# Kernel optimization log

Hardware: AMD Instinct MI355X
Metric: run time of the kernel (lower is better)

The kernel has to match this reference:

```python
import math
import jax, jax.numpy as jnp
import numpy as np

B, H, W = 2, 128, 128
HW = H * W
D, NH, NL, KS = 256, 8, 1, 5
NP = KS * KS
HD = D // NH
DFF = 1024
KEEP = 0.25
H_SIZE = 188.0
EPS = 1e-5


def _layernorm(x, g, b):
    m = x.mean(-1, keepdims=True)
    v = ((x - m) ** 2).mean(-1, keepdims=True)
    return (x - m) * jax.lax.rsqrt(v + EPS) * g + b


def _mha(q_in, k_in, v_in, w_qkv, b_qkv, w_o, b_o):
    wq, wk, wv = jnp.split(w_qkv, 3, axis=0)
    bq, bk, bv = jnp.split(b_qkv, 3, axis=0)
    def heads(x, w, b):
        y = x @ w.T + b
        return y.reshape(y.shape[0], y.shape[1], NH, HD)
    q, k, v = heads(q_in, wq, bq), heads(k_in, wk, bk), heads(v_in, wv, bv)
    scores = jnp.einsum('bqhd,bkhd->bhqk', q, k) / math.sqrt(HD)
    attn = jax.nn.softmax(scores, axis=-1)
    out = jnp.einsum('bhqk,bkhd->bqhd', attn, v).reshape(q_in.shape[0], q_in.shape[1], D)
    return out @ w_o.T + b_o


def _bilinear(v, grid):
    # v: (B, HW, NH, HD); grid: (B, LQ, NH, NP, 2) normalized (x, y) in [0,1]
    x = grid[..., 0] * W - 0.5
    y = grid[..., 1] * H - 0.5
    x0 = jnp.floor(x); y0 = jnp.floor(y)
    lx = x - x0; ly = y - y0
    x0i = x0.astype(jnp.int32); y0i = y0.astype(jnp.int32)
    bidx = jnp.arange(v.shape[0])[:, None, None, None]
    hidx = jnp.arange(NH)[None, None, :, None]
    def corner(xi, yi, wgt):
        valid = (xi >= 0) & (xi < W) & (yi >= 0) & (yi < H)  # zero-pad outside
        idx = jnp.clip(yi, 0, H - 1) * W + jnp.clip(xi, 0, W - 1)
        s = v[bidx, idx, hidx]  # (B, LQ, NH, NP, HD)
        return s * (wgt * valid)[..., None]
    return (corner(x0i, y0i, (1 - lx) * (1 - ly))
            + corner(x0i + 1, y0i, lx * (1 - ly))
            + corner(x0i, y0i + 1, (1 - lx) * ly)
            + corner(x0i + 1, y0i + 1, lx * ly))


def _where_to_attend(query, ref_windows, lbw, lbb, sow, sob, kernel_indices):
    Bq, L = ref_windows.shape[:2]
    ob = (query @ lbw.T + lbb).reshape(Bq, L, NH, NL, 4)  # with_rotation=False -> 4 vars
    rw = ref_windows[:, :, None, None, :]  # (B, L, 1, 1, 7)
    ref_boxes = rw[..., jnp.array([0, 1, 3, 4])]
    ref_angles = rw[..., 6:7]
    angles = jnp.broadcast_to(ref_angles, (Bq, L, NH, NL, 1))
    boxes = ref_boxes + ob / 8.0 * ref_boxes[..., jnp.array([2, 3, 2, 3])]
    center = boxes[..., None, :2]  # (B, L, NH, NL, 1, 2)
    size = boxes[..., None, 2:]
    cos_a, sin_a = jnp.cos(angles), jnp.sin(angles)
    rot = jnp.stack([cos_a, -sin_a, sin_a, cos_a], -1).reshape(Bq, L, NH, NL, 1, 2, 2)
    dgrid = (query @ sow.T + sob).reshape(Bq, L, NH, NL, NP, 2) / H_SIZE
    fg = kernel_indices * jax.nn.relu(size)              # (B, L, NH, NL, NP, 2)
    fg = center + (fg[..., None, :] * rot).sum(-1)       # rotate then shift
    return fg + dgrid


def _box_attn(query, value, ref_windows, vpw, vpb, law, lab, lbw, lbb, sow, sob, ow, ob_, kernel_indices):
    Bq, LQ = query.shape[:2]
    LV = value.shape[1]
    v = (value @ vpw.T + vpb).reshape(Bq, LV, NH, HD)
    aw = jax.nn.softmax((query @ law.T + lab).reshape(Bq, LQ, NH, NL * NP), axis=-1)
    aw = aw.reshape(Bq, LQ, NH, NL, NP)
    grid = _where_to_attend(query, ref_windows, lbw, lbb, sow, sob, kernel_indices)
    sampled = _bilinear(v, grid[:, :, :, 0])             # single level (NL=1)
    out = (aw[:, :, :, 0, :, None] * sampled).sum(-2).reshape(Bq, LQ, D)
    return out @ ow.T + ob_


def _forward(src, pos, ref_windows, score_mask, in_proj_w, in_proj_b, mha_out_w, mha_out_b,
             value_proj_w, value_proj_b, linear_attn_w, linear_attn_b, linear_box_w, linear_box_b,
             samp_off_w, samp_off_b, ca_out_w, ca_out_b, lin1_w, lin1_b, lin2_w, lin2_b,
             qn_g, qn_b, n1_g, n1_b, n2_g, n2_b, kernel_indices):
    Bq = src.shape[0]
    fg_num = math.ceil(src.shape[1] * KEEP)
    sel_score, indices = jax.lax.top_k(score_mask, fg_num)
    gather = lambda x, i: jnp.take_along_axis(x, i[..., None], axis=1)
    sel_src = gather(src, indices)
    sel_pos = gather(pos, indices)
    sel_ref = gather(ref_windows, indices)
    q_num = math.ceil(fg_num * KEEP)
    q_idx = jax.lax.top_k(sel_score, q_num)[1]
    q_src = gather(sel_src, q_idx)
    q_pos = gather(sel_pos, q_idx)
    qk = q_src + q_pos
    q2 = _mha(qk, qk, q_src, in_proj_w, in_proj_b, mha_out_w, mha_out_b)
    q_src = _layernorm(q_src + q2, qn_g, qn_b)
    brow = jnp.arange(Bq)[:, None]
    sel_src = sel_src.at[brow, q_idx].set(q_src)
    src2 = _box_attn(sel_src + sel_pos, src, sel_ref, value_proj_w, value_proj_b,
                     linear_attn_w, linear_attn_b, linear_box_w, linear_box_b,
                     samp_off_w, samp_off_b, ca_out_w, ca_out_b, kernel_indices)
    sel_src = _layernorm(sel_src + src2, n1_g, n1_b)
    ff = jax.nn.relu(sel_src @ lin1_w.T + lin1_b) @ lin2_w.T + lin2_b
    sel_src = _layernorm(sel_src + ff, n2_g, n2_b)
    return src.at[brow, indices].set(sel_src)


def setup_inputs() -> dict:
    key = jax.random.key(0)
    ks = jax.random.split(key, 16)
    def w(k, shape):
        return jax.random.normal(k, shape, dtype=jnp.float32) * 0.02
    # deformable sampling-offsets bias init (per-head directional grid)
    thetas = np.arange(NH) * (2.0 * np.pi / NH)
    g = np.stack([np.cos(thetas), np.sin(thetas)], -1)
    g = g / np.abs(g).max(-1, keepdims=True)
    g = np.tile(g.reshape(NH, 1, 1, 2), (1, NL, NP, 1)) * (np.arange(NP) + 1).reshape(1, 1, NP, 1)
    samp_off_b = jnp.asarray(g.reshape(-1), dtype=jnp.float32)
    # fixed kernel indices buffer (odd kernel, (x,y) order, /kernel_size)
    ind = np.linspace(-(KS - 1) / 2, (KS - 1) / 2, KS)
    ii, jj = np.meshgrid(ind, ind, indexing='ij')
    kernel_indices = jnp.asarray(np.stack([jj, ii], -1).reshape(-1, 2) / KS, dtype=jnp.float32)
    return dict(
        src=jax.random.normal(ks[0], (B, HW, D), dtype=jnp.float32),
        pos=jax.random.normal(ks[1], (B, HW, D), dtype=jnp.float32),
        src_shape=jnp.array([[H, W]], dtype=jnp.int32),
        src_start_idx=jnp.zeros((1,), dtype=jnp.int32),
        ref_windows=jax.random.uniform(ks[2], (B, HW, 7), dtype=jnp.float32),
        score_mask=jax.random.normal(ks[3], (B, HW), dtype=jnp.float32),
        in_proj_w=w(ks[4], (3 * D, D)), in_proj_b=jnp.zeros((3 * D,), jnp.float32),
        mha_out_w=w(ks[5], (D, D)), mha_out_b=jnp.zeros((D,), jnp.float32),
        value_proj_w=w(ks[6], (D, D)), value_proj_b=jnp.zeros((D,), jnp.float32),
        linear_attn_w=w(ks[7], (NH * NL * NP, D)), linear_attn_b=jnp.zeros((NH * NL * NP,), jnp.float32),
        linear_box_w=w(ks[8], (NL * NH * 4, D)), linear_box_b=jnp.zeros((NL * NH * 4,), jnp.float32),
        samp_off_w=w(ks[9], (NH * NL * NP * 2, D)), samp_off_b=samp_off_b,
        ca_out_w=w(ks[10], (D, D)), ca_out_b=jnp.zeros((D,), jnp.float32),
        lin1_w=w(ks[11], (DFF, D)), lin1_b=jnp.zeros((DFF,), jnp.float32),
        lin2_w=w(ks[12], (D, DFF)), lin2_b=jnp.zeros((D,), jnp.float32),
        qn_g=jnp.ones((D,), jnp.float32), qn_b=jnp.zeros((D,), jnp.float32),
        n1_g=jnp.ones((D,), jnp.float32), n1_b=jnp.zeros((D,), jnp.float32),
        n2_g=jnp.ones((D,), jnp.float32), n2_b=jnp.zeros((D,), jnp.float32),
        kernel_indices=kernel_indices,
    )


def reference(src, pos, src_shape, src_start_idx, ref_windows, score_mask,
              in_proj_w, in_proj_b, mha_out_w, mha_out_b, value_proj_w, value_proj_b,
              linear_attn_w, linear_attn_b, linear_box_w, linear_box_b, samp_off_w, samp_off_b,
              ca_out_w, ca_out_b, lin1_w, lin1_b, lin2_w, lin2_b,
              qn_g, qn_b, n1_g, n1_b, n2_g, n2_b, kernel_indices):
    # src_shape/src_start_idx are static single-level metadata (H, W closed over)
    return _forward(src, pos, ref_windows, score_mask, in_proj_w, in_proj_b, mha_out_w, mha_out_b,
                    value_proj_w, value_proj_b, linear_attn_w, linear_attn_b, linear_box_w, linear_box_b,
                    samp_off_w, samp_off_b, ca_out_w, ca_out_b, lin1_w, lin1_b, lin2_w, lin2_b,
                    qn_g, qn_b, n1_g, n1_b, n2_g, n2_b, kernel_indices)
```

## Files before the change

kernel.cpp:

```cpp
#include <hip/hip_runtime.h>
#include <hip/hip_bf16.h>
#include <math.h>

#define HW_N   16384
#define DIM    256
#define NSEL   4096
#define NQ     1024
#define NHEAD  8
#define HD     32
#define NP_    25
#define DFF_   1024

#define OFF_SELREF  8448LL
#define OFF_SELSRC  65792LL
#define OFF_SELPOS  2162944LL
#define OFF_QUERY   4260096LL
#define OFF_BIG     6357248LL
#define OFF_WBF     10551552LL
#define OFF_F       14745856LL

__device__ __forceinline__ unsigned int f2s(float f) {
    unsigned int u = __float_as_uint(f);
    return (u & 0x80000000u) ? ~u : (u | 0x80000000u);
}

typedef __bf16 bf16x8 __attribute__((ext_vector_type(8)));
typedef __bf16 bf16x4 __attribute__((ext_vector_type(4)));
typedef float  f32x4  __attribute__((ext_vector_type(4)));

extern "C" __global__ __launch_bounds__(256)
void wcvt_kernel(const float* __restrict__ s0, const float* __restrict__ s1,
                 const float* __restrict__ s2, const float* __restrict__ s3,
                 const float* __restrict__ s4, const float* __restrict__ s5,
                 const float* __restrict__ s6, const float* __restrict__ s7,
                 const float* __restrict__ s8, __hip_bfloat16* __restrict__ dst) {
    const long long g = (long long)blockIdx.x * 256 + threadIdx.x;
    const float* s; long long base;
    if      (g < 196608)  { s = s0; base = 0; }
    else if (g < 262144)  { s = s1; base = 196608; }
    else if (g < 327680)  { s = s2; base = 262144; }
    else if (g < 378880)  { s = s3; base = 327680; }
    else if (g < 387072)  { s = s4; base = 378880; }
    else if (g < 489472)  { s = s5; base = 387072; }
    else if (g < 555008)  { s = s6; base = 489472; }
    else if (g < 817152)  { s = s7; base = 555008; }
    else                  { s = s8; base = 817152; }
    dst[g] = __float2bfloat16(s[g - base]);
}

extern "C" __global__ __launch_bounds__(512)
void topk_hist_kernel(const float* __restrict__ score, unsigned int* __restrict__ hist) {
    const int t = threadIdx.x, bx = blockIdx.x, bb = blockIdx.y;
    const int i = bx * 512 + t;
    unsigned int u = f2s(score[(long long)bb * HW_N + i]);
    atomicAdd(&hist[bb * 8192 + (u >> 19)], 1u);
}

extern "C" __global__ __launch_bounds__(1024)
void topk_scan_kernel(const unsigned int* __restrict__ hist, unsigned int* __restrict__ ctrl) {
    __shared__ unsigned int scan[1024];
    const int t = threadIdx.x, bb = blockIdx.x;
    unsigned int loc[8]; unsigned int lsum = 0u;
    #pragma unroll
    for (int k = 0; k < 8; ++k) { loc[k] = hist[bb * 8192 + t * 8 + k]; lsum += loc[k]; }
    scan[t] = lsum;
    __syncthreads();
    for (int off = 1; off < 1024; off <<= 1) {
        unsigned int v = (t + off < 1024) ? scan[t + off] : 0u;
        __syncthreads();
        scan[t] += v;
        __syncthreads();
    }
    unsigned int nxt = (t < 1023) ? scan[t + 1] : 0u;
    unsigned int run = nxt;
    for (int k = 7; k >= 0; --k) {
        run += loc[k];
        unsigned int above = run - loc[k];
        if (run >= 1024u && above < 1024u) { ctrl[bb * 16 + 0] = (unsigned)(t * 8 + k); ctrl[bb * 16 + 1] = 1024u - above; }
        if (run >= 4096u && above < 4096u) { ctrl[bb * 16 + 2] = (unsigned)(t * 8 + k); ctrl[bb * 16 + 3] = 4096u - above; }
    }
}

extern "C" __global__ __launch_bounds__(1024)
void topk_collect_kernel(const float* __restrict__ score, unsigned int* __restrict__ ctrl,
                         unsigned long long* __restrict__ list1,
                         unsigned long long* __restrict__ list2) {
    const int t = threadIdx.x, bx = blockIdx.x, bb = blockIdx.y;
    const int i = bx * 1024 + t;
    const unsigned int T1 = ctrl[bb * 16 + 0], T2 = ctrl[bb * 16 + 2];
    unsigned int u = f2s(score[(long long)bb * HW_N + i]);
    unsigned int bin = u >> 19;
    unsigned long long key = ((unsigned long long)u << 32) | (unsigned int)(~(unsigned int)i);
    if (bin == T1) {
        unsigned int p = atomicAdd(&ctrl[bb * 16 + 4], 1u);
        if (p < 2048u) list1[bb * 2048 + p] = key;
    }
    if (bin == T2 && T2 != T1) {
        unsigned int p = atomicAdd(&ctrl[bb * 16 + 5], 1u);
        if (p < 2048u) list2[bb * 2048 + p] = key;
    }
}

extern "C" __global__ __launch_bounds__(1024)
void topk_classify_kernel(const float* __restrict__ score, unsigned int* __restrict__ ctrl,
                          const unsigned long long* __restrict__ list1,
                          const unsigned long long* __restrict__ list2,
                          int* __restrict__ idx_out) {
    __shared__ unsigned int cA, cB, baseA, baseB;
    const int t = threadIdx.x, bx = blockIdx.x, bb = blockIdx.y;
    const int i = bx * 1024 + t;
    if (t == 0) { cA = 0u; cB = 0u; }
    __syncthreads();
    const unsigned int T1 = ctrl[bb * 16 + 0], need1 = ctrl[bb * 16 + 1];
    const unsigned int T2 = ctrl[bb * 16 + 2], need2 = ctrl[bb * 16 + 3];
    const unsigned int c1 = min(ctrl[bb * 16 + 4], 2048u);
    const unsigned int c2 = min(ctrl[bb * 16 + 5], 2048u);
    unsigned int u = f2s(score[(long long)bb * HW_N + i]);
    unsigned int bin = u >> 19;
    unsigned long long key = ((unsigned long long)u << 32) | (unsigned int)(~(unsigned int)i);
    bool inA = false, inB = false;
    if (bin > T1) {
        inA = true;
    } else if (bin == T1) {
        unsigned int r = 0;
        for (unsigned int q = 0; q < c1; ++q) r += (list1[bb * 2048 + q] > key) ? 1u : 0u;
        if (r < need1) inA = true;
        else if (T2 == T1) inB = (r < need2);
        else inB = true;
    } else if (bin > T2) {
        inB = true;
    } else if (bin == T2) {
        unsigned int r = 0;
        for (unsigned int q = 0; q < c2; ++q) r += (list2[bb * 2048 + q] > key) ? 1u : 0u;
        inB = (r < need2);
    }
    unsigned int sA = 0u, sB = 0u;
    if (inA) sA = atomicAdd(&cA, 1u);
    if (inB) sB = atomicAdd(&cB, 1u);
    __syncthreads();
    if (t == 0) {
        baseA = atomicAdd(&ctrl[bb * 16 + 6], cA);
        baseB = atomicAdd(&ctrl[bb * 16 + 7], cB);
    }
    __syncthreads();
    if (inA) idx_out[bb * NSEL + baseA + sA] = i;
    if (inB) idx_out[bb * NSEL + 1024 + baseB + sB] = i;
}

extern "C" __global__ __launch_bounds__(256)
void gather_kernel(const float* __restrict__ src, const float* __restrict__ pos,
                   const float* __restrict__ refw, const int* __restrict__ idx,
                   float* __restrict__ selsrc, float* __restrict__ selpos,
                   float* __restrict__ selref, float* __restrict__ qk) {
    const int s = blockIdx.x, bb = blockIdx.y, t = threadIdx.x;
    const int i = idx[bb * NSEL + s];
    const long long so = ((long long)(bb * NSEL + s)) * DIM;
    const long long go = ((long long)(bb * HW_N + i)) * DIM;
    float sv = src[go + t], pv = pos[go + t];
    selsrc[so + t] = sv;
    selpos[so + t] = pv;
    if (s < NQ) qk[((long long)(bb * NQ + s)) * DIM + t] = sv + pv;
    if (t < 7)
        selref[(long long)(bb * NSEL + s) * 7 + t] = refw[(long long)(bb * HW_N + i) * 7 + t];
}

extern "C" __global__ __launch_bounds__(256)
void gemm_kernel(const void* __restrict__ Avp, long long sA,
                 const __hip_bfloat16* __restrict__ W, const float* __restrict__ bias,
                 float* __restrict__ C, long long sC,
                 int M, int N, int K, int relu, int omode, int amode) {
    __shared__ __hip_bfloat16 As[64][72];
    __shared__ __hip_bfloat16 Ws[64][72];
    const int t = threadIdx.x;
    const int n0 = blockIdx.x * 64, m0 = blockIdx.y * 64;
    const long long zoff = (long long)blockIdx.z * sC;
    const int lane = t & 63, wv = t >> 6;
    const int mw = (wv >> 1) * 32, nw = (wv & 1) * 32;
    const int fr = lane & 15;
    const int fk = (lane >> 4) * 8;
    const int sr = t >> 2;
    const int sk = (t & 3) * 16;

    f32x4 acc[2][2];
    #pragma unroll
    for (int i = 0; i < 2; ++i)
        #pragma unroll
        for (int j = 0; j < 2; ++j) acc[i][j] = {0.f, 0.f, 0.f, 0.f};

    const bool wok = (n0 + sr) < N;
    for (int k0 = 0; k0 < K; k0 += 64) {
        uint4 wa = make_uint4(0u, 0u, 0u, 0u), wb = make_uint4(0u, 0u, 0u, 0u);
        if (wok) {
            const __hip_bfloat16* wp = W + (long long)(n0 + sr) * K + k0 + sk;
            wa = *(const uint4*)wp;
            wb = *(const uint4*)(wp + 8);
        }
        if (amode) {
            const __hip_bfloat16* ap = (const __hip_bfloat16*)Avp
                + (long long)blockIdx.z * sA + (long long)(m0 + sr) * K + k0 + sk;
            uint4 aa = *(const uint4*)ap;
            uint4 ab = *(const uint4*)(ap + 8);
            __syncthreads();
            *(uint4*)&As[sr][sk] = aa;
            *(uint4*)&As[sr][sk + 8] = ab;
            *(uint4*)&Ws[sr][sk] = wa;
            *(uint4*)&Ws[sr][sk + 8] = wb;
        } else {
            const float* ap = (const float*)Avp
                + (long long)blockIdx.z * sA + (long long)(m0 + sr) * K + k0 + sk;
            float av[16];
            #pragma unroll
            for (int q = 0; q < 4; ++q) {
                float4 v = *(const float4*)(ap + q * 4);
                av[q * 4 + 0] = v.x; av[q * 4 + 1] = v.y; av[q * 4 + 2] = v.z; av[q * 4 + 3] = v.w;
            }
            __syncthreads();
            #pragma unroll
            for (int q = 0; q < 16; ++q) As[sr][sk + q] = __float2bfloat16(av[q]);
            *(uint4*)&Ws[sr][sk] = wa;
            *(uint4*)&Ws[sr][sk + 8] = wb;
        }
        __syncthreads();
        #pragma unroll
        for (int kk = 0; kk < 64; kk += 32) {
            bf16x8 a0 = *(const bf16x8*)&As[mw + fr][kk + fk];
            bf16x8 a1 = *(const bf16x8*)&As[mw + 16 + fr][kk + fk];
            bf16x8 b0 = *(const bf16x8*)&Ws[nw + fr][kk + fk];
            bf16x8 b1 = *(const bf16x8*)&Ws[nw + 16 + fr][kk + fk];
            acc[0][0] = __builtin_amdgcn_mfma_f32_16x16x32_bf16(a0, b0, acc[0][0], 0, 0, 0);
            acc[0][1] = __builtin_amdgcn_mfma_f32_16x16x32_bf16(a0, b1, acc[0][1], 0, 0, 0);
            acc[1][0] = __builtin_amdgcn_mfma_f32_16x16x32_bf16(a1, b0, acc[1][0], 0, 0, 0);
            acc[1][1] = __builtin_amdgcn_mfma_f32_16x16x32_bf16(a1, b1, acc[1][1], 0, 0, 0);
        }
    }
    const int crow = (lane >> 4) * 4;
    #pragma unroll
    for (int mi = 0; mi < 2; ++mi) {
        #pragma unroll
        for (int ni = 0; ni < 2; ++ni) {
            const int col = n0 + nw + ni * 16 + fr;
            if (col < N) {
                const float bv = bias ? bias[col] : 0.f;
                #pragma unroll
                for (int r = 0; r < 4; ++r) {
                    const int row = m0 + mw + mi * 16 + crow + r;
                    float v = acc[mi][ni][r] + bv;
                    if (relu) v = fmaxf(v, 0.f);
                    if (omode == 0) {
                        C[zoff + (long long)row * N + col] = v;
                    } else if (omode == 1) {
                        ((__hip_bfloat16*)C)[zoff + (long long)row * N + col] = __float2bfloat16(v);
                    } else if (omode == 2) {
                        ((__hip_bfloat16*)C)[zoff + (long long)col * M + row] = __float2bfloat16(v);
                    } else {
                        ((__hip_bfloat16*)C)[zoff + ((long long)(col >> 5) * 16384 + row) * 32 + (col & 31)]
                            = __float2bfloat16(v);
                    }
                }
            }
        }
    }
}

extern "C" __global__ __launch_bounds__(256, 4)
void attn_kernel(const __hip_bfloat16* __restrict__ qkb,
                 const __hip_bfloat16* __restrict__ vT,
                 float* __restrict__ attout) {
    __shared__ float sbuf[8256];
    __shared__ float redm[4][16];
    __shared__ float reds[4][16];
    __hip_bfloat16 (*pb)[1032] = (__hip_bfloat16 (*)[1032])sbuf;
    float (*redo)[16][33] = (float (*)[16][33])sbuf;
    const int t = threadIdx.x;
    const int qt = blockIdx.x, h = blockIdx.y, bb = blockIdx.z;
    const int q0 = qt * 16;
    const int lane = t & 63, wv = t >> 6;
    const int fr = lane & 15, g = lane >> 4;
    const int kbase = wv * 256;
    const float scale = 0.17677669529663687f;

    bf16x8 qfrag = *(const bf16x8*)(qkb + ((long long)(bb * NQ + q0 + fr)) * 512 + h * HD + g * 8);

    f32x4 sfr[16];
    #pragma unroll
    for (int half = 0; half < 2; ++half) {
        bf16x8 kf[8];
        #pragma unroll
        for (int j = 0; j < 8; ++j) {
            const int key0 = kbase + (half * 8 + j) * 16;
            kf[j] = *(const bf16x8*)(qkb + ((long long)(bb * NQ + key0 + fr)) * 512 + 256 + h * HD + g * 8);
        }
        __builtin_amdgcn_sched_barrier(0);
        #pragma unroll
        for (int j = 0; j < 8; ++j) {
            f32x4 z = {0.f, 0.f, 0.f, 0.f};
            sfr[half * 8 + j] = __builtin_amdgcn_mfma_f32_16x16x32_bf16(qfrag, kf[j], z, 0, 0, 0);
        }
    }
    #pragma unroll
    for (int kt = 0; kt < 16; ++kt)
        #pragma unroll
        for (int r = 0; r < 4; ++r) sfr[kt][r] *= scale;

    float mxr[4];
    #pragma unroll
    for (int r = 0; r < 4; ++r) {
        float mx = -1e30f;
        #pragma unroll
        for (int kt = 0; kt < 16; ++kt) mx = fmaxf(mx, sfr[kt][r]);
        #pragma unroll
        for (int mm = 1; mm <= 8; mm <<= 1) mx = fmaxf(mx, __shfl_xor(mx, mm, 64));
        float sm = 0.f;
        #pragma unroll
        for (int kt = 0; kt < 16; ++kt) {
            float e = __expf(sfr[kt][r] - mx);
            sfr[kt][r] = e;
            sm += e;
        }
        #pragma unroll
        for (int mm = 1; mm <= 8; mm <<= 1) sm += __shfl_xor(sm, mm, 64);
        mxr[r] = mx;
        if (fr == 0) { redm[wv][4 * g + r] = mx; reds[wv][4 * g + r] = sm; }
    }
    __syncthreads();

    float scl[4];
    #pragma unroll
    for (int r = 0; r < 4; ++r) {
        const int q = 4 * g + r;
        float mm = fmaxf(fmaxf(redm[0][q], redm[1][q]), fmaxf(redm[2][q], redm[3][q]));
        float ll = 0.f;
        #pragma unroll
        for (int w2 = 0; w2 < 4; ++w2) ll += reds[w2][q] * __expf(redm[w2][q] - mm);
        scl[r] = __expf(mxr[r] - mm) / ll;
    }
    #pragma unroll
    for (int kt = 0; kt < 16; ++kt) {
        #pragma unroll
        for (int r = 0; r < 4; ++r) {
            pb[4 * g + r][kbase + kt * 16 + fr] = __float2bfloat16(sfr[kt][r] * scl[r]);
        }
    }

    f32x4 o0 = {0.f, 0.f, 0.f, 0.f}, o1 = {0.f, 0.f, 0.f, 0.f};
    const __hip_bfloat16* vbase = vT + ((long long)bb * DIM + h * HD) * 1024;
    #pragma unroll
    for (int ksb = 0; ksb < 2; ++ksb) {
        bf16x8 pf[4], v0[4], v1[4];
        #pragma unroll
        for (int j = 0; j < 4; ++j) {
            const int key0 = kbase + (ksb * 4 + j) * 32 + g * 8;
            pf[j] = *(const bf16x8*)&pb[fr][key0];
            v0[j] = *(const bf16x8*)(vbase + (long long)fr * 1024 + key0);
            v1[j] = *(const bf16x8*)(vbase + (long long)(16 + fr) * 1024 + key0);
        }
        __builtin_amdgcn_sched_barrier(0);
        #pragma unroll
        for (int j = 0; j < 4; ++j) {
            o0 = __builtin_amdgcn_mfma_f32_16x16x32_bf16(pf[j], v0[j], o0, 0, 0, 0);
            o1 = __builtin_amdgcn_mfma_f32_16x16x32_bf16(pf[j], v1[j], o1, 0, 0, 0);
        }
    }

    __syncthreads();
    #pragma unroll
    for (int r = 0; r < 4; ++r) {
        redo[wv][4 * g + r][fr] = o0[r];
        redo[wv][4 * g + r][16 + fr] = o1[r];
    }
    __syncthreads();
    #pragma unroll
    for (int i = 0; i < 2; ++i) {
        const int idx = t + i * 256;
        const int q = idx >> 5, d = idx & 31;
        float v = redo[0][q][d] + redo[1][q][d] + redo[2][q][d] + redo[3][q][d];
        attout[((long long)(bb * NQ + q0 + q)) * DIM + h * HD + d] = v;
    }
}

extern "C" __global__ __launch_bounds__(256)
void ln_kernel(const float* __restrict__ X, long long sx,
               const float* __restrict__ R, long long sr,
               const float* __restrict__ g, const float* __restrict__ bta,
               float* __restrict__ O, long long so) {
    __shared__ float red[4];
    const int row = blockIdx.x, bb = blockIdx.y, t = threadIdx.x;
    float x = X[(long long)bb * sx + (long long)row * DIM + t]
            + R[(long long)bb * sr + (long long)row * DIM + t];
    float v = x;
    #pragma unroll
    for (int m = 32; m >= 1; m >>= 1) v += __shfl_xor(v, m, 64);
    if ((t & 63) == 0) red[t >> 6] = v;
    __syncthreads();
    float mean = (red[0] + red[1] + red[2] + red[3]) * (1.f / 256.f);
    __syncthreads();
    float d = x - mean;
    v = d * d;
    #pragma unroll
    for (int m = 32; m >= 1; m >>= 1) v += __shfl_xor(v, m, 64);
    if ((t & 63) == 0) red[t >> 6] = v;
    __syncthreads();
    float var = (red[0] + red[1] + red[2] + red[3]) * (1.f / 256.f);
    O[(long long)bb * so + (long long)row * DIM + t] = d * rsqrtf(var + 1e-5f) * g[t] + bta[t];
}

extern "C" __global__ __launch_bounds__(256)
void addq_kernel(const float* __restrict__ a, const float* __restrict__ b2, float* __restrict__ o) {
    long long i = (long long)blockIdx.x * 256 + threadIdx.x;
    o[i] = a[i] + b2[i];
}

extern "C" __global__ __launch_bounds__(256)
void boxattn_kernel(const float* __restrict__ aw, const float* __restrict__ ob,
                    const float* __restrict__ dgrid, const float* __restrict__ selref,
                    const __hip_bfloat16* __restrict__ vp, const float* __restrict__ kidx,
                    float* __restrict__ boxout) {
    __shared__ float aw_s[200];
    __shared__ float ob_s[32];
    __shared__ float ref_s[7];
    __shared__ float ki_s[50];
    __shared__ float box_s[8][6];
    __shared__ float mx_s[8];
    __shared__ float inv_s[8];
    __shared__ float wq_s[200];
    __shared__ int   i4_s[800];
    __shared__ float w4_s[800];
    __shared__ float red4[4][8][33];
    const int t = threadIdx.x;
    const int s = blockIdx.x, bb = blockIdx.y;
    const long long base = (long long)(bb * NSEL + s);
    if (t < 200) aw_s[t] = aw[base * 200 + t];
    if (t < 32)  ob_s[t] = ob[base * 32 + t];
    if (t < 7)   ref_s[t] = selref[base * 7 + t];
    if (t < 50)  ki_s[t] = kidx[t];
    __syncthreads();

    if (t < 8) {
        float mx = -1e30f;
        #pragma unroll
        for (int p = 0; p < NP_; ++p) mx = fmaxf(mx, aw_s[t * NP_ + p]);
        mx_s[t] = mx;
        const float r0 = ref_s[0], r1 = ref_s[1], r3 = ref_s[3], r4 = ref_s[4], r6 = ref_s[6];
        box_s[t][0] = r0 + ob_s[t * 4 + 0] * 0.125f * r3;
        box_s[t][1] = r1 + ob_s[t * 4 + 1] * 0.125f * r4;
        box_s[t][2] = fmaxf(r3 + ob_s[t * 4 + 2] * 0.125f * r3, 0.f);
        box_s[t][3] = fmaxf(r4 + ob_s[t * 4 + 3] * 0.125f * r4, 0.f);
        box_s[t][4] = cosf(r6);
        box_s[t][5] = sinf(r6);
    }
    __syncthreads();

    if (t < 200) {
        const int h = t / NP_, p = t - h * NP_;
        const float w = expf(aw_s[t] - mx_s[h]);
        wq_s[t] = w;
        const float cx = box_s[h][0], cy = box_s[h][1];
        const float sw = box_s[h][2], sh = box_s[h][3];
        const float ca = box_s[h][4], sa = box_s[h][5];
        const float fx = ki_s[p * 2 + 0] * sw;
        const float fy = ki_s[p * 2 + 1] * sh;
        const float gx = cx + ca * fx - sa * fy + dgrid[base * 400 + 2 * t + 0] * (1.f / 188.f);
        const float gy = cy + sa * fx + ca * fy + dgrid[base * 400 + 2 * t + 1] * (1.f / 188.f);
        const float x = gx * 128.f - 0.5f;
        const float y = gy * 128.f - 0.5f;
        const float x0f = floorf(x), y0f = floorf(y);
        const float lx = x - x0f, ly = y - y0f;
        const int x0 = (int)x0f, y0 = (int)y0f;
        #pragma unroll
        for (int c = 0; c < 4; ++c) {
            const int xi = x0 + (c & 1);
            const int yi = y0 + (c >> 1);
            const float wgt = ((c & 1) ? lx : 1.f - lx) * ((c >> 1) ? ly : 1.f - ly);
            const bool valid = (xi >= 0) & (xi < 128) & (yi >= 0) & (yi < 128);
            const int cxi = min(max(xi, 0), 127);
            const int cyi = min(max(yi, 0), 127);
            i4_s[t * 4 + c] = cyi * 128 + cxi;
            w4_s[t * 4 + c] = w * (valid ? wgt : 0.f);
        }
    }
    __syncthreads();
    if (t < 8) {
        float sm = 0.f;
        #pragma unroll
        for (int p = 0; p < NP_; ++p) sm += wq_s[t * NP_ + p];
        inv_s[t] = 1.f / sm;
    }

    {
        const int lane = t & 63, wv = t >> 6;
        const int h2 = lane >> 3;
        const int j2 = (lane >> 2) & 1;
        const int q2 = lane & 3;
        const int stream = wv * 2 + j2;
        const __hip_bfloat16* vb = vp + ((long long)(bb * 8 + h2) * 16384) * 32 + q2 * 8;
        float a[8] = {0.f, 0.f, 0.f, 0.f, 0.f, 0.f, 0.f, 0.f};
        #pragma unroll
        for (int u = 0; u < 13; ++u) {
            const int j = stream + u * 8;
            const bool ok = (j < 100);
            const int e = h2 * 100 + (ok ? j : 0);
            bf16x8 v = *(const bf16x8*)(vb + (long long)i4_s[e] * 32);
            const float w = ok ? w4_s[e] : 0.f;
            #pragma unroll
            for (int k = 0; k < 8; ++k) a[k] += w * (float)v[k];
        }
        #pragma unroll
        for (int k = 0; k < 8; ++k) a[k] += __shfl_xor(a[k], 4, 64);
        if (j2 == 0) {
            #pragma unroll
            for (int k = 0; k < 8; ++k) red4[wv][h2][q2 * 8 + k] = a[k];
        }
    }
    __syncthreads();
    {
        const int h = t >> 5, d = t & 31;
        float v = red4[0][h][d] + red4[1][h][d] + red4[2][h][d] + red4[3][h][d];
        boxout[base * DIM + h * HD + d] = v * inv_s[h];
    }
}

extern "C" __global__ __launch_bounds__(256)
void scatter_kernel(const int* __restrict__ idx, const float* __restrict__ sel,
                    float* __restrict__ out) {
    const int s = blockIdx.x, bb = blockIdx.y, t = threadIdx.x;
    const int i = idx[bb * NSEL + s];
    out[((long long)(bb * HW_N + i)) * DIM + t] = sel[((long long)(bb * NSEL + s)) * DIM + t];
}

extern "C" void kernel_launch(void* const* d_in, const int* in_sizes, int n_in,
                              void* d_out, int out_size, void* d_ws, size_t ws_size,
                              hipStream_t stream) {
    const float* src          = (const float*)d_in[0];
    const float* pos          = (const float*)d_in[1];
    const float* refw         = (const float*)d_in[4];
    const float* score        = (const float*)d_in[5];
    const float* in_proj_w    = (const float*)d_in[6];
    const float* in_proj_b    = (const float*)d_in[7];
    const float* mha_out_w    = (const float*)d_in[8];
    const float* mha_out_b    = (const float*)d_in[9];
    const float* value_proj_w = (const float*)d_in[10];
    const float* value_proj_b = (const float*)d_in[11];
    const float* lin_attn_w   = (const float*)d_in[12];
    const float* lin_attn_b   = (const float*)d_in[13];
    const float* lin_box_w    = (const float*)d_in[14];
    const float* lin_box_b    = (const float*)d_in[15];
    const float* samp_off_w   = (const float*)d_in[16];
    const float* samp_off_b   = (const float*)d_in[17];
    const float* ca_out_w     = (const float*)d_in[18];
    const float* ca_out_b     = (const float*)d_in[19];
    const float* lin1_w       = (const float*)d_in[20];
    const float* lin1_b       = (const float*)d_in[21];
    const float* lin2_w       = (const float*)d_in[22];
    const float* lin2_b       = (const float*)d_in[23];
    const float* qn_g         = (const float*)d_in[24];
    const float* qn_b         = (const float*)d_in[25];
    const float* n1_g         = (const float*)d_in[26];
    const float* n1_b         = (const float*)d_in[27];
    const float* n2_g         = (const float*)d_in[28];
    const float* n2_b         = (const float*)d_in[29];
    const float* kidx         = (const float*)d_in[30];

    float* w = (float*)d_ws;
    int* idxp = (int*)d_ws;
    float* selref = w + OFF_SELREF;
    float* selsrc = w + OFF_SELSRC;
    float* selpos = w + OFF_SELPOS;
    float* boxout = w + OFF_SELPOS;
    float* query  = w + OFF_QUERY;
    float* src2   = w + OFF_QUERY;
    __hip_bfloat16* vproj  = (__hip_bfloat16*)(w + OFF_BIG);
    __hip_bfloat16* ffntb  = (__hip_bfloat16*)(w + OFF_BIG);
    __hip_bfloat16* wbf    = (__hip_bfloat16*)(w + OFF_WBF);
    float* qk     = w + OFF_F;
    __hip_bfloat16* qkb = (__hip_bfloat16*)(w + OFF_F + 524288);
    __hip_bfloat16* vT  = (__hip_bfloat16*)(w + OFF_F + 1572864);
    float* attout = w + OFF_F + 2097152;
    float* q2     = w + OFF_F + 2621440;
    float* aw     = w + OFF_F;
    float* obuf   = w + OFF_F + 1638400;
    float* dgrid  = w + OFF_F + 1900544;
    float* ff     = w + OFF_F;
    unsigned int* hist2 = (unsigned int*)(w + OFF_F);
    unsigned int* ctrl2 = hist2 + 16384;
    unsigned long long* list1 = (unsigned long long*)(hist2 + 16448);
    unsigned long long* list2 = list1 + 2 * 2048;
    float* out    = (float*)d_out;

    const long long W_INPROJ = 0, W_MHAOUT = 196608, W_VALUE = 262144,
                    W_LATTN = 327680, W_LBOX = 378880, W_SOFF = 387072,
                    W_CAOUT = 489472, W_LIN1 = 555008, W_LIN2 = 817152;

    hipMemcpyAsync(d_out, src, (size_t)2 * HW_N * DIM * sizeof(float),
                   hipMemcpyDeviceToDevice, stream);

    wcvt_kernel<<<4216, 256, 0, stream>>>(in_proj_w, mha_out_w, value_proj_w,
                                          lin_attn_w, lin_box_w, samp_off_w,
                                          ca_out_w, lin1_w, lin2_w, wbf);

    hipMemsetAsync(hist2, 0, 16448 * sizeof(unsigned int), stream);
    topk_hist_kernel<<<dim3(32, 2), 512, 0, stream>>>(score, hist2);
    topk_scan_kernel<<<2, 1024, 0, stream>>>(hist2, ctrl2);
    topk_collect_kernel<<<dim3(16, 2), 1024, 0, stream>>>(score, ctrl2, list1, list2);
    topk_classify_kernel<<<dim3(16, 2), 1024, 0, stream>>>(score, ctrl2, list1, list2, idxp);

    gather_kernel<<<dim3(NSEL, 2), 256, 0, stream>>>(src, pos, refw, idxp,
                                                     selsrc, selpos, selref, qk);
    gemm_kernel<<<dim3(8, 16, 2), 256, 0, stream>>>(qk, 262144LL, wbf + W_INPROJ, in_proj_b,
                                                    (float*)qkb, 524288LL, NQ, 512, 256, 0, 1, 0);
    gemm_kernel<<<dim3(4, 16, 2), 256, 0, stream>>>(selsrc, 1048576LL, wbf + W_INPROJ + 512 * 256,
                                                    in_proj_b + 512, (float*)vT, 262144LL, NQ, 256, 256, 0, 2, 0);
    attn_kernel<<<dim3(64, 8, 2), 256, 0, stream>>>(qkb, vT, attout);
    gemm_kernel<<<dim3(4, 16, 2), 256, 0, stream>>>(attout, 262144LL, wbf + W_MHAOUT, mha_out_b,
                                                    q2, 262144LL, NQ, 256, 256, 0, 0, 0);
    ln_kernel<<<dim3(NQ, 2), 256, 0, stream>>>(selsrc, 1048576LL, q2, 262144LL,
                                               qn_g, qn_b, selsrc, 1048576LL);
    addq_kernel<<<8192, 256, 0, stream>>>(selsrc, selpos, query);
    gemm_kernel<<<dim3(4, 256, 2), 256, 0, stream>>>(src, 4194304LL, wbf + W_VALUE, value_proj_b,
                                                     (float*)vproj, 4194304LL, HW_N, 256, 256, 0, 3, 0);
    gemm_kernel<<<dim3(4, 64, 2), 256, 0, stream>>>(query, 1048576LL, wbf + W_LATTN, lin_attn_b,
                                                    aw, 819200LL, NSEL, 200, 256, 0, 0, 0);
    gemm_kernel<<<dim3(1, 64, 2), 256, 0, stream>>>(query, 1048576LL, wbf + W_LBOX, lin_box_b,
                                                    obuf, 131072LL, NSEL, 32, 256, 0, 0, 0);
    gemm_kernel<<<dim3(7, 64, 2), 256, 0, stream>>>(query, 1048576LL, wbf + W_SOFF, samp_off_b,
                                                    dgrid, 1638400LL, NSEL, 400, 256, 0, 0, 0);
    boxattn_kernel<<<dim3(NSEL, 2), 256, 0, stream>>>(aw, obuf, dgrid, selref, vproj, kidx, boxout);
    gemm_kernel<<<dim3(4, 64, 2), 256, 0, stream>>>(boxout, 1048576LL, wbf + W_CAOUT, ca_out_b,
                                                    src2, 1048576LL, NSEL, 256, 256, 0, 0, 0);
    ln_kernel<<<dim3(NSEL, 2), 256, 0, stream>>>(selsrc, 1048576LL, src2, 1048576LL,
                                                 n1_g, n1_b, selsrc, 1048576LL);
    gemm_kernel<<<dim3(16, 64, 2), 256, 0, stream>>>(selsrc, 1048576LL, wbf + W_LIN1, lin1_b,
                                                     (float*)ffntb, 4194304LL, NSEL, DFF_, 256, 1, 1, 0);
    gemm_kernel<<<dim3(4, 64, 2), 256, 0, stream>>>(ffntb, 4194304LL, wbf + W_LIN2, lin2_b,
                                                    ff, 1048576LL, NSEL, 256, DFF_, 0, 0, 1);
    ln_kernel<<<dim3(NSEL, 2), 256, 0, stream>>>(selsrc, 1048576LL, ff, 1048576LL,
                                                 n2_g, n2_b, selsrc, 1048576LL);
    scatter_kernel<<<dim3(NSEL, 2), 256, 0, stream>>>(idxp, selsrc, out);
}
```

Before: 437.2 us.

## Remap box-attention blocks to one head over sixteen queries

The box-attention kernel now runs one block per (batch, head) pair for sixteen selected queries, instead of one block per query covering all heads. Sampling offsets are staged into shared memory with the other per-query inputs. Each block then gathers from a single head's value plane, which should improve L2 locality of the bilinear gathers and cut the block count. The final reduction uses cross-lane shuffles and vectorized float4 stores instead of a shared-memory reduction, and exp is switched to the fast intrinsic, at some cost in precision.

```diff
diff --git a/kernel.cpp b/kernel.cpp
--- a/kernel.cpp
+++ b/kernel.cpp
@@ -415,32 +415,45 @@
                     const float* __restrict__ dgrid, const float* __restrict__ selref,
                     const __hip_bfloat16* __restrict__ vp, const float* __restrict__ kidx,
                     float* __restrict__ boxout) {
-    __shared__ float aw_s[200];
-    __shared__ float ob_s[32];
-    __shared__ float ref_s[7];
+    __shared__ float aw_s[400];
+    __shared__ float ob_s[64];
+    __shared__ float ref_s[112];
     __shared__ float ki_s[50];
-    __shared__ float box_s[8][6];
-    __shared__ float mx_s[8];
-    __shared__ float inv_s[8];
-    __shared__ float wq_s[200];
-    __shared__ int   i4_s[800];
-    __shared__ float w4_s[800];
-    __shared__ float red4[4][8][33];
+    __shared__ float dg_s[800];
+    __shared__ float box_s[16][6];
+    __shared__ float mx_s[16];
+    __shared__ float inv_s[16];
+    __shared__ float wq_s[400];
+    __shared__ int   i4_s[1600];
+    __shared__ float w4_s[1600];
     const int t = threadIdx.x;
-    const int s = blockIdx.x, bb = blockIdx.y;
-    const long long base = (long long)(bb * NSEL + s);
-    if (t < 200) aw_s[t] = aw[base * 200 + t];
-    if (t < 32)  ob_s[t] = ob[base * 32 + t];
-    if (t < 7)   ref_s[t] = selref[base * 7 + t];
+    const int combo = blockIdx.x;
+    const int bb = combo >> 3, h = combo & 7;
+    const int s0 = blockIdx.y * 16;
+    const long long base = (long long)bb * NSEL + s0;
+
+    #pragma unroll
+    for (int e = t; e < 400; e += 256) {
+        const int s = e / 25, p = e - s * 25;
+        aw_s[e] = aw[(base + s) * 200 + h * 25 + p];
+    }
+    if (t < 64)  ob_s[t] = ob[(base + (t >> 2)) * 32 + h * 4 + (t & 3)];
+    if (t < 112) ref_s[t] = selref[base * 7 + t];
     if (t < 50)  ki_s[t] = kidx[t];
-    __syncthreads();
-
-    if (t < 8) {
+    #pragma unroll
+    for (int e = t; e < 800; e += 256) {
+        const int s = e / 50, r = e - s * 50;
+        dg_s[e] = dgrid[(base + s) * 400 + h * 50 + r];
+    }
+    __syncthreads();
+
+    if (t < 16) {
         float mx = -1e30f;
         #pragma unroll
         for (int p = 0; p < NP_; ++p) mx = fmaxf(mx, aw_s[t * NP_ + p]);
         mx_s[t] = mx;
-        const float r0 = ref_s[0], r1 = ref_s[1], r3 = ref_s[3], r4 = ref_s[4], r6 = ref_s[6];
+        const float r0 = ref_s[t * 7 + 0], r1 = ref_s[t * 7 + 1];
+        const float r3 = ref_s[t * 7 + 3], r4 = ref_s[t * 7 + 4], r6 = ref_s[t * 7 + 6];
         box_s[t][0] = r0 + ob_s[t * 4 + 0] * 0.125f * r3;
         box_s[t][1] = r1 + ob_s[t * 4 + 1] * 0.125f * r4;
         box_s[t][2] = fmaxf(r3 + ob_s[t * 4 + 2] * 0.125f * r3, 0.f);
@@ -450,17 +463,18 @@
     }
     __syncthreads();
 
-    if (t < 200) {
-        const int h = t / NP_, p = t - h * NP_;
-        const float w = expf(aw_s[t] - mx_s[h]);
-        wq_s[t] = w;
-        const float cx = box_s[h][0], cy = box_s[h][1];
-        const float sw = box_s[h][2], sh = box_s[h][3];
-        const float ca = box_s[h][4], sa = box_s[h][5];
+    #pragma unroll
+    for (int e = t; e < 400; e += 256) {
+        const int s = e / 25, p = e - s * 25;
+        const float w = __expf(aw_s[e] - mx_s[s]);
+        wq_s[e] = w;
+        const float cx = box_s[s][0], cy = box_s[s][1];
+        const float sw = box_s[s][2], sh = box_s[s][3];
+        const float ca = box_s[s][4], sa = box_s[s][5];
         const float fx = ki_s[p * 2 + 0] * sw;
         const float fy = ki_s[p * 2 + 1] * sh;
-        const float gx = cx + ca * fx - sa * fy + dgrid[base * 400 + 2 * t + 0] * (1.f / 188.f);
-        const float gy = cy + sa * fx + ca * fy + dgrid[base * 400 + 2 * t + 1] * (1.f / 188.f);
+        const float gx = cx + ca * fx - sa * fy + dg_s[s * 50 + 2 * p + 0] * (1.f / 188.f);
+        const float gy = cy + sa * fx + ca * fy + dg_s[s * 50 + 2 * p + 1] * (1.f / 188.f);
         const float x = gx * 128.f - 0.5f;
         const float y = gy * 128.f - 0.5f;
         const float x0f = floorf(x), y0f = floorf(y);
@@ -474,12 +488,13 @@
             const bool valid = (xi >= 0) & (xi < 128) & (yi >= 0) & (yi < 128);
             const int cxi = min(max(xi, 0), 127);
             const int cyi = min(max(yi, 0), 127);
-            i4_s[t * 4 + c] = cyi * 128 + cxi;
-            w4_s[t * 4 + c] = w * (valid ? wgt : 0.f);
-        }
-    }
-    __syncthreads();
-    if (t < 8) {
+            i4_s[e * 4 + c] = cyi * 128 + cxi;
+            w4_s[e * 4 + c] = w * (valid ? wgt : 0.f);
+        }
+    }
+    __syncthreads();
+
+    if (t < 16) {
         float sm = 0.f;
         #pragma unroll
         for (int p = 0; p < NP_; ++p) sm += wq_s[t * NP_ + p];
@@ -487,35 +502,34 @@
     }
 
     {
-        const int lane = t & 63, wv = t >> 6;
-        const int h2 = lane >> 3;
-        const int j2 = (lane >> 2) & 1;
+        const int lane = t & 63;
+        const int s_loc = t >> 4;
+        const int j2 = (lane >> 2) & 3;
         const int q2 = lane & 3;
-        const int stream = wv * 2 + j2;
-        const __hip_bfloat16* vb = vp + ((long long)(bb * 8 + h2) * 16384) * 32 + q2 * 8;
+        const __hip_bfloat16* vb = vp + ((long long)(bb * 8 + h) * 16384) * 32 + q2 * 8;
+        const int ebase = s_loc * 100;
         float a[8] = {0.f, 0.f, 0.f, 0.f, 0.f, 0.f, 0.f, 0.f};
         #pragma unroll
-        for (int u = 0; u < 13; ++u) {
-            const int j = stream + u * 8;
-            const bool ok = (j < 100);
-            const int e = h2 * 100 + (ok ? j : 0);
-            bf16x8 v = *(const bf16x8*)(vb + (long long)i4_s[e] * 32);
-            const float w = ok ? w4_s[e] : 0.f;
+        for (int u = 0; u < 25; ++u) {
+            const int ii = ebase + j2 + 4 * u;
+            bf16x8 v = *(const bf16x8*)(vb + (long long)i4_s[ii] * 32);
+            const float w = w4_s[ii];
             #pragma unroll
             for (int k = 0; k < 8; ++k) a[k] += w * (float)v[k];
         }
         #pragma unroll
         for (int k = 0; k < 8; ++k) a[k] += __shfl_xor(a[k], 4, 64);
+        #pragma unroll
+        for (int k = 0; k < 8; ++k) a[k] += __shfl_xor(a[k], 8, 64);
+        __syncthreads();
         if (j2 == 0) {
-            #pragma unroll
-            for (int k = 0; k < 8; ++k) red4[wv][h2][q2 * 8 + k] = a[k];
-        }
-    }
-    __syncthreads();
-    {
-        const int h = t >> 5, d = t & 31;
-        float v = red4[0][h][d] + red4[1][h][d] + red4[2][h][d] + red4[3][h][d];
-        boxout[base * DIM + h * HD + d] = v * inv_s[h];
+            const float inv = inv_s[s_loc];
+            float* op = boxout + (base + s_loc) * DIM + h * HD + q2 * 8;
+            float4 o0 = {a[0] * inv, a[1] * inv, a[2] * inv, a[3] * inv};
+            float4 o1 = {a[4] * inv, a[5] * inv, a[6] * inv, a[7] * inv};
+            *(float4*)op = o0;
+            *(float4*)(op + 4) = o1;
+        }
     }
 }
 
@@ -623,7 +637,7 @@
                                                     obuf, 131072LL, NSEL, 32, 256, 0, 0, 0);
     gemm_kernel<<<dim3(7, 64, 2), 256, 0, stream>>>(query, 1048576LL, wbf + W_SOFF, samp_off_b,
                                                     dgrid, 1638400LL, NSEL, 400, 256, 0, 0, 0);
-    boxattn_kernel<<<dim3(NSEL, 2), 256, 0, stream>>>(aw, obuf, dgrid, selref, vproj, kidx, boxout);
+    boxattn_kernel<<<dim3(16, 256), 256, 0, stream>>>(aw, obuf, dgrid, selref, vproj, kidx, boxout);
     gemm_kernel<<<dim3(4, 64, 2), 256, 0, stream>>>(boxout, 1048576LL, wbf + W_CAOUT, ca_out_b,
                                                     src2, 1048576LL, NSEL, 256, 256, 0, 0, 0);
     ln_kernel<<<dim3(NSEL, 2), 256, 0, stream>>>(selsrc, 1048576LL, src2, 1048576LL,
```

Result: faster. 419.7 us (-4.0%).
